# Optimization experiments

Hardware: AMD Instinct MI355X
Metric: run time of the kernel (lower is better)

## Reference

```python
import math
import jax, jax.numpy as jnp
import numpy as np

# ---------------- static irrep configuration ----------------
RS_IN = [(16, 0, 0), (16, 1, 0)]
RS_OUT = [(16, 0, 0), (16, 1, 0)]


def selection_rule(l_in, p_in, l_out, p_out):
    return [l for l in range(abs(l_in - l_out), l_in + l_out + 1)
            if p_out == 0 or p_in * (-1) ** l == p_out]


# ---------------- real Wigner 3j (Clebsch-Gordan) ----------------

def _su2_cg(j1, j2, j3, m1, m2, m3):
    if m1 + m2 != m3:
        return 0.0
    f = math.factorial
    pref = math.sqrt((2 * j3 + 1) * f(j3 + j1 - j2) * f(j3 - j1 + j2) * f(j1 + j2 - j3) / f(j1 + j2 + j3 + 1))
    pref *= math.sqrt(f(j3 + m3) * f(j3 - m3) * f(j1 - m1) * f(j1 + m1) * f(j2 - m2) * f(j2 + m2))
    s = 0.0
    for k in range(0, j1 + j2 - j3 + 1):
        d = [k, j1 + j2 - j3 - k, j1 - m1 - k, j2 + m2 - k, j3 - j1 - m2 + k, j3 - j2 + m1 + k]
        if any(x < 0 for x in d):
            continue
        s += (-1) ** k / np.prod([float(f(x)) for x in d])
    return pref * s


def _c2r(l):
    # real SH = A @ complex SH, rows/cols ordered m = -l..l
    A = np.zeros((2 * l + 1, 2 * l + 1), dtype=complex)
    s2 = 1.0 / math.sqrt(2)
    for m in range(-l, l + 1):
        if m < 0:
            A[l + m, l + m] = 1j * s2
            A[l + m, l - m] = -1j * (-1) ** m * s2
        elif m == 0:
            A[l, l] = 1.0
        else:
            A[l + m, l - m] = s2
            A[l + m, l + m] = (-1) ** m * s2
    return A


_W3J_CACHE = {}

def wigner_3j(l1, l2, l3):
    key = (l1, l2, l3)
    if key in _W3J_CACHE:
        return _W3J_CACHE[key]
    C = np.zeros((2 * l1 + 1, 2 * l2 + 1, 2 * l3 + 1))
    for m1 in range(-l1, l1 + 1):
        for m2 in range(-l2, l2 + 1):
            m3 = -(m1 + m2)
            if abs(m3) <= l3:
                C[l1 + m1, l2 + m2, l3 + m3] = ((-1) ** (l1 - l2 - m3) / math.sqrt(2 * l3 + 1)
                                                * _su2_cg(l1, l2, l3, m1, m2, -m3))
    T = np.einsum('ia,jb,kc,abc->ijk', _c2r(l1), _c2r(l2), _c2r(l3), C.astype(complex))
    T = T * (-1j) ** (l1 + l2 + l3)
    re, im = np.real(T), np.imag(T)
    T = re if np.abs(re).sum() >= np.abs(im).sum() else im
    n = math.sqrt(float((T ** 2).sum()))
    T = T / n if n > 1e-12 else T
    _W3J_CACHE[key] = T
    return T


# ---------------- real spherical harmonics (l = 0,1,2) ----------------

def real_sh(ls, xyz):
    r = jnp.linalg.norm(xyz, axis=-1)
    n = xyz / jnp.where(r > 0, r, 1.0)[..., None]
    x, y, z = n[..., 0], n[..., 1], n[..., 2]
    out = []
    for l in ls:
        if l == 0:
            out.append(jnp.full(x.shape, 0.28209479177387814, x.dtype)[None])
        elif l == 1:
            c = 0.4886025119029199
            out.append(jnp.stack([c * y, c * z, c * x]))
        elif l == 2:
            c1 = 1.0925484305920792
            c2 = 0.31539156525252005
            c3 = 0.5462742152960396
            out.append(jnp.stack([c1 * x * y, c1 * y * z, c2 * (3 * z * z - 1), c1 * x * z, c3 * (x * x - y * y)]))
        else:
            raise NotImplementedError
    return jnp.concatenate(out, axis=0)  # [sum(2l+1), batch, a, b]


def _norm_coef_table():
    nc = np.zeros((len(RS_OUT), len(RS_IN), 2))
    for i, (mul_out, l_out, p_out) in enumerate(RS_OUT):
        num = sum(mul_in * len(selection_rule(l_in, p_in, l_out, p_out))
                  for (mul_in, l_in, p_in) in RS_IN)
        for j, (mul_in, l_in, p_in) in enumerate(RS_IN):
            lm = math.sqrt(2 * l_in + 1) * math.sqrt(4 * math.pi)
            nc[i, j, 0] = lm / math.sqrt(num)
            nc[i, j, 1] = lm / math.sqrt(mul_in)
    return nc


def kernel_conv(features, geometry, mask, W1, b1, W2, b2):
    batch, a, b, _ = geometry.shape
    set_of_l_filters = sorted({l for (_, li, pi) in RS_IN for (_, lo, po) in RS_OUT
                               for l in selection_rule(li, pi, lo, po)})
    Y = real_sh(set_of_l_filters, geometry)             # [9, z, a, b]
    radii = jnp.linalg.norm(geometry, axis=-1)          # [z, a, b]
    # radial MLP: 1 -> H -> n_path
    h = jax.nn.relu(radii[..., None] * W1[0] + b1)
    R = h @ W2 + b2                                     # [z, a, b, n_path]
    nc = _norm_coef_table()
    is_zero = radii == 0

    out_blocks = []
    begin_R = 0
    for i, (mul_out, l_out, p_out) in enumerate(RS_OUT):
        block = jnp.zeros((batch, a, mul_out, 2 * l_out + 1), features.dtype)
        begin_in = 0
        for j, (mul_in, l_in, p_in) in enumerate(RS_IN):
            s_in = slice(begin_in, begin_in + mul_in * (2 * l_in + 1))
            begin_in += mul_in * (2 * l_in + 1)
            l_filters = selection_rule(l_in, p_in, l_out, p_out)
            if not l_filters:
                continue
            n = mul_out * mul_in * len(l_filters)
            sub_R = R[..., begin_R:begin_R + n].reshape(batch, a, b, mul_out, mul_in, len(l_filters))
            begin_R += n
            sub_nc = jnp.where(is_zero, nc[i, j, 1], nc[i, j, 0]).astype(features.dtype)
            f_in = features[..., s_in].reshape(batch, b, mul_in, 2 * l_in + 1)
            for k, l_f in enumerate(l_filters):
                offset = sum(2 * l + 1 for l in set_of_l_filters if l < l_f)
                sub_Y = Y[offset:offset + 2 * l_f + 1]
                C = jnp.asarray(wigner_3j(l_out, l_in, l_f), features.dtype)
                block = block + jnp.einsum('ijk,kzab,zabuv,zab,zbvj->zaui',
                                           C, sub_Y, sub_R[..., k], sub_nc, f_in)
        out_blocks.append(block.reshape(batch, a, -1))
    out = jnp.concatenate(out_blocks, axis=-1)          # [z, a, n_out]
    return out * mask[..., None]


def setup_inputs() -> dict:
    key = jax.random.key(0)
    ks = jax.random.split(key, 6)
    batch, a, b = 2, 160, 160
    dim_in, n_path, H = 64, 1536, 64
    return {
        'features': jax.random.normal(ks[0], (batch, b, dim_in), jnp.float32),
        'geometry': jax.random.normal(ks[1], (batch, a, b, 3), jnp.float32),
        'mask': jnp.ones((batch, b), jnp.float32),
        'W1': jax.random.normal(ks[2], (1, H), jnp.float32) * 0.5,
        'b1': jax.random.normal(ks[3], (H,), jnp.float32) * 0.1,
        'W2': jax.random.normal(ks[4], (H, n_path), jnp.float32) / np.sqrt(H),
        'b2': jnp.zeros((n_path,), jnp.float32),
    }


def reference(features, geometry, mask, W1, b1, W2, b2):
    return kernel_conv(features, geometry, mask, W1, b1, W2, b2)
```

## Files before the change

### kernel.cpp

```cpp
#include <hip/hip_runtime.h>
#include <hip/hip_fp16.h>
#include <math.h>

#define NPATH 1536
#define SEGS  65
#define NB    160
#define NA    160
#define CW    32
#define PPW   5

#define PC_U32S   (320 * SEGS * 256)
#define W2G_OFF   PC_U32S
#define B2T_OFF   (W2G_OFF + 256 * 16 * 64)

__device__ float dg_thr[64];
__device__ float dg_iw[64], dg_ib[64], dg_dw[64], dg_db[64];
__device__ int   dg_ord[64];

#define SCL_A 0.17677669529663687f
#define SCL_B 0.6266570686577502f
#define SCL_C 0.2558286876965162f
#define SCL_D 0.125f
#define SCL_E 0.3133285343288751f
#define SCL_F 0.7674950309598664f

static __device__ __forceinline__ void slot_map(int t, int& pbase, int& pstr,
                                                int& comp, float& scl) {
    int lane4 = t >> 2, j = t & 3;
    pbase = 0; pstr = 1; comp = -1; scl = 0.0f;
    if (lane4 < 16) {
        if (j == 0) { pbase = lane4 * 16;       scl = SCL_A; }
        else        { pbase = 256 + lane4 * 16; comp = j - 1; scl = SCL_B; }
    } else {
        int lu = lane4 - 16, u = lu / 3, part = lu - u * 3;
        if (part == 0) {
            if (j == 0) { pbase = 512 + u * 16;                       scl = SCL_C; }
            else        { pbase = 768 + u * 48; pstr = 3; comp = j - 1; scl = SCL_D; }
        } else if (part == 1) {
            if (j < 3)  { pbase = 768 + u * 48 + 1; pstr = 3; comp = j; scl = SCL_E; }
        } else {
            if (j < 3)  { pbase = 768 + u * 48 + 2; pstr = 3; comp = j; scl = SCL_F; }
        }
    }
}

__global__ __launch_bounds__(256) void k_w2g(const float* __restrict__ W1,
                                             const float* __restrict__ b1,
                                             const float* __restrict__ W2,
                                             const float* __restrict__ b2,
                                             float* __restrict__ ws,
                                             float* __restrict__ out) {
    int bid = blockIdx.x, tid = threadIdx.x;
    if (bid == 256) {
        __shared__ float tvL[64];
        if (tid < 64) {
            float w = W1[tid], bb = b1[tid];
            tvL[tid] = (w != 0.0f) ? (-bb / w) : __builtin_inff();
        }
        __syncthreads();
        if (tid < 64) {
            float mine = tvL[tid];
            int rank = 0;
            for (int j2 = 0; j2 < 64; ++j2) {
                float o = tvL[j2];
                rank += (o < mine || (o == mine && j2 < tid)) ? 1 : 0;
            }
            float w = W1[tid], bb = b1[tid];
            dg_iw[tid] = (w < 0.0f) ? w : 0.0f;
            dg_ib[tid] = (w < 0.0f) ? bb : ((w == 0.0f && bb > 0.0f) ? bb : 0.0f);
            dg_ord[rank] = tid;
            dg_dw[rank]  = fabsf(w);
            dg_db[rank]  = (w > 0.0f) ? bb : ((w < 0.0f) ? -bb : 0.0f);
            dg_thr[tid]  = mine;
        }
        return;
    }
    if (bid > 256) {
        out[(bid - 257) * 256 + tid] = 0.0f;
        return;
    }
    int t = bid;
    int pbase, pstr, comp; float scl;
    slot_map(t, pbase, pstr, comp, scl);
    (void)comp;
    int c = tid & 63, vq = tid >> 6;
    float* W2G = ws + W2G_OFF;
    #pragma unroll
    for (int vv = 0; vv < 4; ++vv) {
        int v = vq * 4 + vv;
        float val = scl * W2[(size_t)c * NPATH + pbase + v * pstr];
        W2G[(size_t)((t << 4) + v) * 64 + c] = val;
    }
    if (tid < 16) {
        ws[B2T_OFF + tid * 256 + t] = scl * b2[pbase + tid * pstr];
    }
}

__global__ __launch_bounds__(128) void k_pc2(const float* __restrict__ feat,
                                             const float* __restrict__ ws,
                                             unsigned int* __restrict__ PC) {
    int bid = blockIdx.x;
    int zb = bid >> 1, half = bid & 1;
    int tid = threadIdx.x, wv = tid >> 6, lane = tid & 63;

    __shared__ float hL[64][129];
    __shared__ float fL[64], iwS[64], ibS[64], dwS[64], dbS[64];
    __shared__ int   ordS[64];

    if (tid < 64) {
        fL[tid]  = feat[(size_t)zb * 64 + tid];
        iwS[tid] = dg_iw[tid];  ibS[tid] = dg_ib[tid];
        dwS[tid] = dg_dw[tid];  dbS[tid] = dg_db[tid];
        ordS[tid] = dg_ord[tid];
    }
    __syncthreads();

    const float* W2G = ws + W2G_OFF;
    #pragma unroll 2
    for (int i = 0; i < 64; ++i) {
        int lt = wv * 64 + i;
        int t  = half * 128 + lt;
        int pbase, pstr, comp; float scl;
        slot_map(t, pbase, pstr, comp, scl);
        (void)pbase; (void)pstr; (void)scl;
        const float* wp = W2G + ((size_t)t << 10) + lane;
        float h = 0.0f;
        #pragma unroll
        for (int v = 0; v < 16; ++v) {
            float fvv = (comp < 0) ? fL[v] : fL[16 + 3 * v + comp];
            h = fmaf(wp[v << 6], fvv, h);
        }
        hL[lane][lt] = h;
    }
    __syncthreads();

    int t = half * 128 + tid;
    int pbase, pstr, comp; float scl;
    slot_map(t, pbase, pstr, comp, scl);
    (void)pbase; (void)pstr; (void)scl;

    float ib2 = 0.0f;
    #pragma unroll
    for (int v = 0; v < 16; ++v) {
        float fvv = (comp < 0) ? fL[v] : fL[16 + 3 * v + comp];
        ib2 = fmaf(ws[B2T_OFF + v * 256 + t], fvv, ib2);
    }

    float slope = 0.0f, icpt = ib2;
    #pragma unroll 4
    for (int c = 0; c < 64; ++c) {
        float h = hL[c][tid];
        slope = fmaf(iwS[c], h, slope);
        icpt  = fmaf(ibS[c], h, icpt);
    }

    unsigned int* rowp = PC + (size_t)zb * (SEGS * 256) + t;
    union { __half2 h; unsigned int u; } pk;
    pk.h = __halves2half2(__float2half(slope), __float2half(icpt));
    rowp[0] = pk.u;
    for (int s = 1; s < SEGS; ++s) {
        float h = hL[ordS[s - 1]][tid];
        slope = fmaf(dwS[s - 1], h, slope);
        icpt  = fmaf(dbS[s - 1], h, icpt);
        pk.h = __halves2half2(__float2half(slope), __float2half(icpt));
        rowp[(size_t)s * 256] = pk.u;
    }
}

static __device__ __forceinline__ float rcomb(unsigned int v, float r) {
    union { unsigned int u; __half2 h; } cv; cv.u = v;
    return fmaf(r, __low2float(cv.h), __high2float(cv.h));
}

__global__ __launch_bounds__(256, 4) void k_main(const float* __restrict__ geom,
                                                 const float* __restrict__ mask,
                                                 const unsigned int* __restrict__ PC,
                                                 float* __restrict__ out) {
    int wv   = threadIdx.x >> 6;
    int lane = threadIdx.x & 63;
    int gw   = blockIdx.x * 4 + wv;
    int chunk = gw & (CW - 1);
    int za    = gw >> 5;
    int z     = za / NA;

    __shared__ float sAcc[4][64];

    bool l0 = lane < 16;
    int  u = 0, part = 0;
    if (!l0) { int lu = lane - 16; u = lu / 3; part = lu - u * 3; }
    float zft = l0 ? 1.4142135623730951f : 2.0f;
    float thrv = dg_thr[lane];

    const float is30 = 0.18257418583505536f;
    const float is10 = 0.31622776601683794f;
    const float c1sh = 0.4886025119029199f;
    const float c21 = 1.0925484305920792f, c22 = 0.31539156525252005f, c23 = 0.5462742152960396f;

    int b0 = chunk * PPW;
    float rr[PPW], nxa[PPW], nya[PPW], nza[PPW], zfa[PPW];
    unsigned int rowo[PPW];
    #pragma unroll
    for (int it = 0; it < PPW; ++it) {
        const float* g = geom + ((size_t)za * NB + b0 + it) * 3;
        float gx = g[0], gy = g[1], gz = g[2];
        float r = sqrtf(gx * gx + gy * gy + gz * gz);
        bool zr = (r == 0.0f);
        float inv = zr ? 1.0f : (1.0f / r);
        nxa[it] = gx * inv; nya[it] = gy * inv; nza[it] = gz * inv;
        rr[it] = r;
        zfa[it] = zr ? zft : 1.0f;
        unsigned long long bm = __ballot(thrv < r);
        int s = __popcll(bm);
        rowo[it] = ((unsigned)(z * NB + b0 + it) * SEGS + (unsigned)s) * 256u
                 + (unsigned)(lane * 4);
    }

    float acc0 = 0.0f, acc1 = 0.0f, acc2 = 0.0f;

    uint4 tb[2];
    tb[0] = *(const uint4*)(PC + rowo[0]);

    #pragma unroll
    for (int it = 0; it < PPW; ++it) {
        if (it + 1 < PPW) tb[(it + 1) & 1] = *(const uint4*)(PC + rowo[it + 1]);
        uint4 tt = tb[it & 1];
        float r = rr[it];
        float T0 = rcomb(tt.x, r);
        float T1 = rcomb(tt.y, r);
        float T2 = rcomb(tt.z, r);
        float T3 = rcomb(tt.w, r);

        float nx = nxa[it], ny = nya[it], nz = nza[it];
        float Y1_0 = c1sh * ny, Y1_1 = c1sh * nz, Y1_2 = c1sh * nx;
        float zf = zfa[it];

        if (l0) {
            float sl0 = T0;
            sl0 = fmaf(Y1_0, T1, sl0);
            sl0 = fmaf(Y1_1, T2, sl0);
            sl0 = fmaf(Y1_2, T3, sl0);
            acc0 = fmaf(sl0, zf, acc0);
        } else if (part == 0) {
            float px = fmaf(Y1_0, T0, T1);
            float py = fmaf(Y1_1, T0, T2);
            float pz = fmaf(Y1_2, T0, T3);
            acc0 = fmaf(px, zf, acc0);
            acc1 = fmaf(py, zf, acc1);
            acc2 = fmaf(pz, zf, acc2);
        } else if (part == 1) {
            float px = fmaf(Y1_2, T1, -Y1_1 * T2);
            float py = fmaf(Y1_0, T2, -Y1_2 * T0);
            float pz = fmaf(Y1_1, T0, -Y1_0 * T1);
            acc0 = fmaf(px, zf, acc0);
            acc1 = fmaf(py, zf, acc1);
            acc2 = fmaf(pz, zf, acc2);
        } else {
            float Y2_0 = c21 * nx * ny;
            float Y2_1 = c21 * ny * nz;
            float Y2_2 = c22 * fmaf(3.0f, nz * nz, -1.0f);
            float Y2_3 = c21 * nx * nz;
            float Y2_4 = c23 * (nx * nx - ny * ny);
            float za_ = is10 * Y2_0, zb_ = is10 * Y2_1, zc_ = is10 * Y2_3;
            float zd_ = is30 * Y2_2, ze_ = is10 * Y2_4;
            float px = fmaf(-(zd_ + ze_), T0, fmaf(zb_, T1, za_ * T2));
            float py = fmaf(zb_, T0, fmaf(2.0f * zd_, T1, zc_ * T2));
            float pz = fmaf(za_, T0, fmaf(zc_, T1, (ze_ - zd_) * T2));
            acc0 = fmaf(px, zf, acc0);
            acc1 = fmaf(py, zf, acc1);
            acc2 = fmaf(pz, zf, acc2);
        }
    }

    float ax = acc0 + __shfl_down(acc0, 1) + __shfl_down(acc0, 2);
    float ay = acc1 + __shfl_down(acc1, 1) + __shfl_down(acc1, 2);
    float az = acc2 + __shfl_down(acc2, 1) + __shfl_down(acc2, 2);
    if (l0) {
        sAcc[wv][lane] = acc0;
    } else if (part == 0) {
        int ob = 16 + u * 3;
        sAcc[wv][ob]     = ax;
        sAcc[wv][ob + 1] = ay;
        sAcc[wv][ob + 2] = az;
    }
    __syncthreads();
    if (threadIdx.x < 64) {
        float sum = sAcc[0][threadIdx.x] + sAcc[1][threadIdx.x]
                  + sAcc[2][threadIdx.x] + sAcc[3][threadIdx.x];
        sum *= mask[za];
        atomicAdd(&out[(size_t)za * 64 + threadIdx.x], sum);
    }
}

extern "C" void kernel_launch(void* const* d_in, const int* in_sizes, int n_in,
                              void* d_out, int out_size, void* d_ws, size_t ws_size,
                              hipStream_t stream) {
    (void)in_sizes; (void)n_in; (void)ws_size; (void)out_size;
    const float* feat = (const float*)d_in[0];
    const float* geom = (const float*)d_in[1];
    const float* mask = (const float*)d_in[2];
    const float* W1   = (const float*)d_in[3];
    const float* b1   = (const float*)d_in[4];
    const float* W2   = (const float*)d_in[5];
    const float* b2   = (const float*)d_in[6];
    float* out = (float*)d_out;
    float* ws  = (float*)d_ws;
    unsigned int* PC = (unsigned int*)d_ws;

    k_w2g<<<337, 256, 0, stream>>>(W1, b1, W2, b2, ws, out);
    k_pc2<<<640, 128, 0, stream>>>(feat, ws, PC);
    k_main<<<2 * NA * CW / 4, 256, 0, stream>>>(geom, mask, PC, out);
}
```

Baseline: 111.6 us.

## Precontract W1/b1 piecewise segments with W2 before multiplying by features

```diff
diff --git a/kernel.cpp b/kernel.cpp
--- a/kernel.cpp
+++ b/kernel.cpp
@@ -10,12 +10,9 @@
 #define PPW   5
 
 #define PC_U32S   (320 * SEGS * 256)
-#define W2G_OFF   PC_U32S
-#define B2T_OFF   (W2G_OFF + 256 * 16 * 64)
+#define SWB_OFF   PC_U32S
 
 __device__ float dg_thr[64];
-__device__ float dg_iw[64], dg_ib[64], dg_dw[64], dg_db[64];
-__device__ int   dg_ord[64];
 
 #define SCL_A 0.17677669529663687f
 #define SCL_B 0.6266570686577502f
@@ -44,126 +41,137 @@
     }
 }
 
-__global__ __launch_bounds__(256) void k_w2g(const float* __restrict__ W1,
-                                             const float* __restrict__ b1,
-                                             const float* __restrict__ W2,
-                                             const float* __restrict__ b2,
-                                             float* __restrict__ ws,
-                                             float* __restrict__ out) {
+__global__ __launch_bounds__(128) void k_sw(const float* __restrict__ W1,
+                                            const float* __restrict__ b1,
+                                            const float* __restrict__ W2,
+                                            const float* __restrict__ b2,
+                                            float* __restrict__ ws,
+                                            float* __restrict__ out) {
     int bid = blockIdx.x, tid = threadIdx.x;
-    if (bid == 256) {
-        __shared__ float tvL[64];
-        if (tid < 64) {
-            float w = W1[tid], bb = b1[tid];
-            tvL[tid] = (w != 0.0f) ? (-bb / w) : __builtin_inff();
-        }
-        __syncthreads();
-        if (tid < 64) {
-            float mine = tvL[tid];
-            int rank = 0;
-            for (int j2 = 0; j2 < 64; ++j2) {
-                float o = tvL[j2];
-                rank += (o < mine || (o == mine && j2 < tid)) ? 1 : 0;
-            }
-            float w = W1[tid], bb = b1[tid];
-            dg_iw[tid] = (w < 0.0f) ? w : 0.0f;
-            dg_ib[tid] = (w < 0.0f) ? bb : ((w == 0.0f && bb > 0.0f) ? bb : 0.0f);
-            dg_ord[rank] = tid;
-            dg_dw[rank]  = fabsf(w);
-            dg_db[rank]  = (w > 0.0f) ? bb : ((w < 0.0f) ? -bb : 0.0f);
-            dg_thr[tid]  = mine;
-        }
+    if (bid >= 256) {
+        out[(bid - 256) * 128 + tid] = 0.0f;
         return;
     }
-    if (bid > 256) {
-        out[(bid - 257) * 256 + tid] = 0.0f;
-        return;
-    }
     int t = bid;
+
+    __shared__ float tvS[64], iwS[64], ibS[64], dwS[64], dbS[64], b2S[16];
+    __shared__ int   ordS[64];
+    __shared__ float W2t[16][65];
+
+    if (tid < 64) {
+        float w = W1[tid], bb = b1[tid];
+        tvS[tid] = (w != 0.0f) ? (-bb / w) : __builtin_inff();
+    }
+    __syncthreads();
+    if (tid < 64) {
+        float mine = tvS[tid];
+        int rank = 0;
+        for (int j2 = 0; j2 < 64; ++j2) {
+            float o = tvS[j2];
+            rank += (o < mine || (o == mine && j2 < tid)) ? 1 : 0;
+        }
+        float w = W1[tid], bb = b1[tid];
+        iwS[tid] = (w < 0.0f) ? w : 0.0f;
+        ibS[tid] = (w < 0.0f) ? bb : ((w == 0.0f && bb > 0.0f) ? bb : 0.0f);
+        ordS[rank] = tid;
+        dwS[rank]  = fabsf(w);
+        dbS[rank]  = (w > 0.0f) ? bb : ((w < 0.0f) ? -bb : 0.0f);
+        if (t == 0) dg_thr[tid] = mine;
+    }
+
     int pbase, pstr, comp; float scl;
     slot_map(t, pbase, pstr, comp, scl);
     (void)comp;
-    int c = tid & 63, vq = tid >> 6;
-    float* W2G = ws + W2G_OFF;
+
+    int c = tid & 63, vh = tid >> 6;
     #pragma unroll
-    for (int vv = 0; vv < 4; ++vv) {
-        int v = vq * 4 + vv;
-        float val = scl * W2[(size_t)c * NPATH + pbase + v * pstr];
-        W2G[(size_t)((t << 4) + v) * 64 + c] = val;
-    }
+    for (int i = 0; i < 8; ++i) {
+        int v = vh * 8 + i;
+        W2t[v][c] = scl * W2[(size_t)c * NPATH + pbase + v * pstr];
+    }
+    if (tid < 16) b2S[tid] = scl * b2[pbase + tid * pstr];
+    __syncthreads();
+
     if (tid < 16) {
-        ws[B2T_OFF + tid * 256 + t] = scl * b2[pbase + tid * pstr];
-    }
-}
-
-__global__ __launch_bounds__(128) void k_pc2(const float* __restrict__ feat,
+        int v = tid;
+        float sw = 0.0f, sb = 0.0f;
+        #pragma unroll 4
+        for (int cc = 0; cc < 64; ++cc) {
+            float w2 = W2t[v][cc];
+            sw = fmaf(iwS[cc], w2, sw);
+            sb = fmaf(ibS[cc], w2, sb);
+        }
+        sb += b2S[v];
+        float2* rp = (float2*)(ws + SWB_OFF + (size_t)t * SEGS * 32) + v;
+        *rp = make_float2(sw, sb);
+        for (int s = 1; s < SEGS; ++s) {
+            int cs = ordS[s - 1];
+            float w2 = W2t[v][cs];
+            sw = fmaf(dwS[s - 1], w2, sw);
+            sb = fmaf(dbS[s - 1], w2, sb);
+            rp += 16;
+            *rp = make_float2(sw, sb);
+        }
+    }
+}
+
+__global__ __launch_bounds__(256) void k_pc3(const float* __restrict__ feat,
                                              const float* __restrict__ ws,
                                              unsigned int* __restrict__ PC) {
-    int bid = blockIdx.x;
-    int zb = bid >> 1, half = bid & 1;
-    int tid = threadIdx.x, wv = tid >> 6, lane = tid & 63;
-
-    __shared__ float hL[64][129];
-    __shared__ float fL[64], iwS[64], ibS[64], dwS[64], dbS[64];
-    __shared__ int   ordS[64];
-
-    if (tid < 64) {
-        fL[tid]  = feat[(size_t)zb * 64 + tid];
-        iwS[tid] = dg_iw[tid];  ibS[tid] = dg_ib[tid];
-        dwS[tid] = dg_dw[tid];  dbS[tid] = dg_db[tid];
-        ordS[tid] = dg_ord[tid];
+    int tg = blockIdx.x & 15, zt = blockIdx.x >> 4;
+    int zb0 = zt * 20;
+
+    __shared__ __align__(16) float fS[20][64];
+    #pragma unroll
+    for (int i = 0; i < 5; ++i) {
+        int idx = threadIdx.x + i * 256;
+        int row = idx >> 6, fi = idx & 63;
+        float val = feat[(size_t)(zb0 + row) * 64 + fi];
+        int dest;
+        if (fi < 16) dest = fi;
+        else { int q = (fi - 16) / 3, c3 = (fi - 16) - 3 * q; dest = (c3 + 1) * 16 + q; }
+        fS[row][dest] = val;
     }
     __syncthreads();
 
-    const float* W2G = ws + W2G_OFF;
-    #pragma unroll 2
-    for (int i = 0; i < 64; ++i) {
-        int lt = wv * 64 + i;
-        int t  = half * 128 + lt;
-        int pbase, pstr, comp; float scl;
-        slot_map(t, pbase, pstr, comp, scl);
-        (void)pbase; (void)pstr; (void)scl;
-        const float* wp = W2G + ((size_t)t << 10) + lane;
-        float h = 0.0f;
-        #pragma unroll
-        for (int v = 0; v < 16; ++v) {
-            float fvv = (comp < 0) ? fL[v] : fL[16 + 3 * v + comp];
-            h = fmaf(wp[v << 6], fvv, h);
-        }
-        hL[lane][lt] = h;
-    }
-    __syncthreads();
-
-    int t = half * 128 + tid;
+    int t = threadIdx.x & 15, sgrp = threadIdx.x >> 4;
+    int T = tg * 16 + t;
     int pbase, pstr, comp; float scl;
-    slot_map(t, pbase, pstr, comp, scl);
+    slot_map(T, pbase, pstr, comp, scl);
     (void)pbase; (void)pstr; (void)scl;
-
-    float ib2 = 0.0f;
-    #pragma unroll
-    for (int v = 0; v < 16; ++v) {
-        float fvv = (comp < 0) ? fL[v] : fL[16 + 3 * v + comp];
-        ib2 = fmaf(ws[B2T_OFF + v * 256 + t], fvv, ib2);
-    }
-
-    float slope = 0.0f, icpt = ib2;
-    #pragma unroll 4
-    for (int c = 0; c < 64; ++c) {
-        float h = hL[c][tid];
-        slope = fmaf(iwS[c], h, slope);
-        icpt  = fmaf(ibS[c], h, icpt);
-    }
-
-    unsigned int* rowp = PC + (size_t)zb * (SEGS * 256) + t;
-    union { __half2 h; unsigned int u; } pk;
-    pk.h = __halves2half2(__float2half(slope), __float2half(icpt));
-    rowp[0] = pk.u;
-    for (int s = 1; s < SEGS; ++s) {
-        float h = hL[ordS[s - 1]][tid];
-        slope = fmaf(dwS[s - 1], h, slope);
-        icpt  = fmaf(dbS[s - 1], h, icpt);
-        pk.h = __halves2half2(__float2half(slope), __float2half(icpt));
-        rowp[(size_t)s * 256] = pk.u;
+    const float* fb = &fS[0][(comp + 1) * 16];
+
+    for (int k = 0; k < 5; ++k) {
+        int s = sgrp + 16 * k;
+        if (s >= SEGS) break;
+        const float4* rp = (const float4*)(ws + SWB_OFF + ((size_t)T * SEGS + s) * 32);
+        float4 q0 = rp[0], q1 = rp[1], q2 = rp[2], q3 = rp[3];
+        float4 q4 = rp[4], q5 = rp[5], q6 = rp[6], q7 = rp[7];
+        unsigned int* op = PC + (size_t)zb0 * (SEGS * 256) + (size_t)s * 256 + T;
+        #pragma unroll 4
+        for (int zb = 0; zb < 20; ++zb) {
+            const float4* fp = (const float4*)(fb + zb * 64);
+            float4 f0 = fp[0], f1 = fp[1], f2 = fp[2], f3 = fp[3];
+            float sw = q0.x * f0.x,          sb = q0.y * f0.x;
+            sw = fmaf(q0.z, f0.y, sw);  sb = fmaf(q0.w, f0.y, sb);
+            sw = fmaf(q1.x, f0.z, sw);  sb = fmaf(q1.y, f0.z, sb);
+            sw = fmaf(q1.z, f0.w, sw);  sb = fmaf(q1.w, f0.w, sb);
+            sw = fmaf(q2.x, f1.x, sw);  sb = fmaf(q2.y, f1.x, sb);
+            sw = fmaf(q2.z, f1.y, sw);  sb = fmaf(q2.w, f1.y, sb);
+            sw = fmaf(q3.x, f1.z, sw);  sb = fmaf(q3.y, f1.z, sb);
+            sw = fmaf(q3.z, f1.w, sw);  sb = fmaf(q3.w, f1.w, sb);
+            sw = fmaf(q4.x, f2.x, sw);  sb = fmaf(q4.y, f2.x, sb);
+            sw = fmaf(q4.z, f2.y, sw);  sb = fmaf(q4.w, f2.y, sb);
+            sw = fmaf(q5.x, f2.z, sw);  sb = fmaf(q5.y, f2.z, sb);
+            sw = fmaf(q5.z, f2.w, sw);  sb = fmaf(q5.w, f2.w, sb);
+            sw = fmaf(q6.x, f3.x, sw);  sb = fmaf(q6.y, f3.x, sb);
+            sw = fmaf(q6.z, f3.y, sw);  sb = fmaf(q6.w, f3.y, sb);
+            sw = fmaf(q7.x, f3.z, sw);  sb = fmaf(q7.y, f3.z, sb);
+            sw = fmaf(q7.z, f3.w, sw);  sb = fmaf(q7.w, f3.w, sb);
+            union { __half2 h; unsigned int u; } pk;
+            pk.h = __halves2half2(__float2half(sw), __float2half(sb));
+            op[(size_t)zb * (SEGS * 256)] = pk.u;
+        }
     }
 }
 
@@ -306,7 +314,7 @@
     float* ws  = (float*)d_ws;
     unsigned int* PC = (unsigned int*)d_ws;
 
-    k_w2g<<<337, 256, 0, stream>>>(W1, b1, W2, b2, ws, out);
-    k_pc2<<<640, 128, 0, stream>>>(feat, ws, PC);
+    k_sw  <<<416, 128, 0, stream>>>(W1, b1, W2, b2, ws, out);
+    k_pc3 <<<256, 256, 0, stream>>>(feat, ws, PC);
     k_main<<<2 * NA * CW / 4, 256, 0, stream>>>(geom, mask, PC, out);
 }
```

Measured after the change: 99.30 us. -11.1%, faster.
